# Performance work log

Hardware: AMD Instinct MI355X
Metric: run time of the kernel (lower is better)

## Reference

```python
import jax, jax.numpy as jnp
import numpy as np

DATA_BITS = 108
SHIFT_BITS = 7


def setup_inputs() -> dict:
    key = jax.random.key(0)
    kx, ks = jax.random.split(key)
    B = 1_000_000
    X = jax.random.randint(kx, (B, DATA_BITS), 0, 2).astype(jnp.float32)
    shift = jax.random.randint(ks, (B, SHIFT_BITS), 0, 2).astype(jnp.int32)
    return {"X": X, "shift": shift}


def reference(X, shift):
    # 7-stage barrel left shift (toward lower indices, MSB-first layout).
    # VecMUX(s, a, b) = s*a + (1-s)*b with s in {0,1}.
    current = X
    s_f = shift.astype(X.dtype)  # [B, 7]
    for layer in range(SHIFT_BITS):
        shift_amt = 2 ** (SHIFT_BITS - 1 - layer)
        if shift_amt >= DATA_BITS:
            shifted = jnp.zeros_like(current)
        else:
            shifted = jnp.concatenate(
                [current[..., shift_amt:], jnp.zeros_like(current[..., :shift_amt])],
                axis=-1,
            )
        s = s_f[..., layer:layer + 1]  # [B, 1]
        current = s * shifted + (1.0 - s) * current
    return current
```

## Files before the change

### kernel.cpp

```cpp
#include <hip/hip_runtime.h>

#define DATA_BITS 108
#define SHIFT_BITS 7
#define F4_PER_ROW 27

__global__ void shift_collapse_kernel(const int* __restrict__ shift,
                                      int* __restrict__ S, int rows) {
    int b = blockIdx.x * blockDim.x + threadIdx.x;
    const int stride = gridDim.x * blockDim.x;
    for (; b < rows; b += stride) {
        const int* p = shift + b * SHIFT_BITS;
        int s = 0;
        #pragma unroll
        for (int l = 0; l < SHIFT_BITS; ++l) {
            s = (s << 1) | (p[l] & 1);
        }
        S[b] = s;
    }
}

__global__ void barrel_shift_kernel(const float* __restrict__ X,
                                    const int* __restrict__ S,
                                    float* __restrict__ out, int total_units) {
    int u = blockIdx.x * blockDim.x + threadIdx.x;
    const int stride = gridDim.x * blockDim.x;
    for (; u < total_units; u += stride) {
        const int b = u / F4_PER_ROW;
        const int q = u - b * F4_PER_ROW;
        const int s = S[b];
        const float* __restrict__ xrow = X + (long long)b * DATA_BITS;
        const int i0 = q * 4;
        float v[4];
        #pragma unroll
        for (int j = 0; j < 4; ++j) {
            const int src = i0 + j + s;
            v[j] = (src < DATA_BITS) ? xrow[src] : 0.0f;
        }
        float4 r = make_float4(v[0], v[1], v[2], v[3]);
        *reinterpret_cast<float4*>(out + (long long)b * DATA_BITS + i0) = r;
    }
}

__global__ void barrel_shift_fused_kernel(const float* __restrict__ X,
                                          const int* __restrict__ shift,
                                          float* __restrict__ out, int total_units) {
    int u = blockIdx.x * blockDim.x + threadIdx.x;
    const int stride = gridDim.x * blockDim.x;
    for (; u < total_units; u += stride) {
        const int b = u / F4_PER_ROW;
        const int q = u - b * F4_PER_ROW;
        const int* p = shift + b * SHIFT_BITS;
        int s = 0;
        #pragma unroll
        for (int l = 0; l < SHIFT_BITS; ++l) s = (s << 1) | (p[l] & 1);
        const float* __restrict__ xrow = X + (long long)b * DATA_BITS;
        const int i0 = q * 4;
        float v[4];
        #pragma unroll
        for (int j = 0; j < 4; ++j) {
            const int src = i0 + j + s;
            v[j] = (src < DATA_BITS) ? xrow[src] : 0.0f;
        }
        float4 r = make_float4(v[0], v[1], v[2], v[3]);
        *reinterpret_cast<float4*>(out + (long long)b * DATA_BITS + i0) = r;
    }
}

extern "C" void kernel_launch(void* const* d_in, const int* in_sizes, int n_in,
                              void* d_out, int out_size, void* d_ws, size_t ws_size,
                              hipStream_t stream) {
    const float* X     = (const float*)d_in[0];
    const int*   shift = (const int*)d_in[1];
    float*       out   = (float*)d_out;

    const int rows = in_sizes[1] / SHIFT_BITS;
    const int total_units = rows * F4_PER_ROW;

    const int block = 256;
    const int grid2 = 2048;

    if (ws_size >= (size_t)rows * sizeof(int)) {
        int* S = (int*)d_ws;
        int grid1 = (rows + block - 1) / block;
        if (grid1 > 2048) grid1 = 2048;
        shift_collapse_kernel<<<grid1, block, 0, stream>>>(shift, S, rows);
        barrel_shift_kernel<<<grid2, block, 0, stream>>>(X, S, out, total_units);
    } else {
        barrel_shift_fused_kernel<<<grid2, block, 0, stream>>>(X, shift, out, total_units);
    }
}
```

Baseline: 149.4 us.

## Fuse shift collapse into tiled barrel kernel with LDS shift cache and nontemporal stores

Replaces the two-kernel scheme (collapse shift bits to a workspace, then gather) with a single kernel. Each 256-thread block handles a tile of 256 rows, decodes their shift amounts into shared memory, and then gathers output float4 units from that shared cache. Output is written with nontemporal stores. This removes one launch and the workspace round trip, and moves from a grid-stride loop to one tile per block, which means many more blocks and a barrier per block.

```diff
diff --git a/kernel.cpp b/kernel.cpp
--- a/kernel.cpp
+++ b/kernel.cpp
@@ -3,66 +3,45 @@
 #define DATA_BITS 108
 #define SHIFT_BITS 7
 #define F4_PER_ROW 27
+#define ROWS_PER_TILE 256
 
-__global__ void shift_collapse_kernel(const int* __restrict__ shift,
-                                      int* __restrict__ S, int rows) {
-    int b = blockIdx.x * blockDim.x + threadIdx.x;
-    const int stride = gridDim.x * blockDim.x;
-    for (; b < rows; b += stride) {
-        const int* p = shift + b * SHIFT_BITS;
+typedef float f32x4 __attribute__((ext_vector_type(4)));
+
+__global__ __launch_bounds__(ROWS_PER_TILE) void barrel_fused_kernel(
+    const float* __restrict__ X,
+    const int* __restrict__ shift,
+    float* __restrict__ out, int rows) {
+    __shared__ int sS[ROWS_PER_TILE];
+
+    const int row0 = blockIdx.x * ROWS_PER_TILE;
+    const int t = threadIdx.x;
+
+    const int r = row0 + t;
+    if (r < rows) {
+        const int* p = shift + r * SHIFT_BITS;
         int s = 0;
         #pragma unroll
-        for (int l = 0; l < SHIFT_BITS; ++l) {
-            s = (s << 1) | (p[l] & 1);
-        }
-        S[b] = s;
+        for (int l = 0; l < SHIFT_BITS; ++l) s = (s << 1) | (p[l] & 1);
+        sS[t] = s;
     }
-}
+    __syncthreads();
 
-__global__ void barrel_shift_kernel(const float* __restrict__ X,
-                                    const int* __restrict__ S,
-                                    float* __restrict__ out, int total_units) {
-    int u = blockIdx.x * blockDim.x + threadIdx.x;
-    const int stride = gridDim.x * blockDim.x;
-    for (; u < total_units; u += stride) {
-        const int b = u / F4_PER_ROW;
-        const int q = u - b * F4_PER_ROW;
-        const int s = S[b];
-        const float* __restrict__ xrow = X + (long long)b * DATA_BITS;
+    const int nrows = min(ROWS_PER_TILE, rows - row0);
+    const int units = nrows * F4_PER_ROW;
+    for (int u = t; u < units; u += ROWS_PER_TILE) {
+        const int rb = u / F4_PER_ROW;
+        const int q  = u - rb * F4_PER_ROW;
+        const int s  = sS[rb];
+        const float* __restrict__ xrow = X + (long long)(row0 + rb) * DATA_BITS;
         const int i0 = q * 4;
-        float v[4];
+        f32x4 v;
         #pragma unroll
         for (int j = 0; j < 4; ++j) {
             const int src = i0 + j + s;
             v[j] = (src < DATA_BITS) ? xrow[src] : 0.0f;
         }
-        float4 r = make_float4(v[0], v[1], v[2], v[3]);
-        *reinterpret_cast<float4*>(out + (long long)b * DATA_BITS + i0) = r;
-    }
-}
-
-__global__ void barrel_shift_fused_kernel(const float* __restrict__ X,
-                                          const int* __restrict__ shift,
-                                          float* __restrict__ out, int total_units) {
-    int u = blockIdx.x * blockDim.x + threadIdx.x;
-    const int stride = gridDim.x * blockDim.x;
-    for (; u < total_units; u += stride) {
-        const int b = u / F4_PER_ROW;
-        const int q = u - b * F4_PER_ROW;
-        const int* p = shift + b * SHIFT_BITS;
-        int s = 0;
-        #pragma unroll
-        for (int l = 0; l < SHIFT_BITS; ++l) s = (s << 1) | (p[l] & 1);
-        const float* __restrict__ xrow = X + (long long)b * DATA_BITS;
-        const int i0 = q * 4;
-        float v[4];
-        #pragma unroll
-        for (int j = 0; j < 4; ++j) {
-            const int src = i0 + j + s;
-            v[j] = (src < DATA_BITS) ? xrow[src] : 0.0f;
-        }
-        float4 r = make_float4(v[0], v[1], v[2], v[3]);
-        *reinterpret_cast<float4*>(out + (long long)b * DATA_BITS + i0) = r;
+        f32x4* dst = reinterpret_cast<f32x4*>(out + (long long)(row0 + rb) * DATA_BITS + i0);
+        __builtin_nontemporal_store(v, dst);
     }
 }
 
@@ -74,18 +53,7 @@
     float*       out   = (float*)d_out;
 
     const int rows = in_sizes[1] / SHIFT_BITS;
-    const int total_units = rows * F4_PER_ROW;
+    const int grid = (rows + ROWS_PER_TILE - 1) / ROWS_PER_TILE;
 
-    const int block = 256;
-    const int grid2 = 2048;
-
-    if (ws_size >= (size_t)rows * sizeof(int)) {
-        int* S = (int*)d_ws;
-        int grid1 = (rows + block - 1) / block;
-        if (grid1 > 2048) grid1 = 2048;
-        shift_collapse_kernel<<<grid1, block, 0, stream>>>(shift, S, rows);
-        barrel_shift_kernel<<<grid2, block, 0, stream>>>(X, S, out, total_units);
-    } else {
-        barrel_shift_fused_kernel<<<grid2, block, 0, stream>>>(X, shift, out, total_units);
-    }
+    barrel_fused_kernel<<<grid, ROWS_PER_TILE, 0, stream>>>(X, shift, out, rows);
 }
```

After: 147.0 us. No clear change (-1.6%).
